# Optimization experiments

Hardware: AMD Instinct MI355X
Metric: run time of the kernel (lower is better)

Reference implementation:

```python
import jax, jax.numpy as jnp
import numpy as np

ALPHA = 0.0

def setup_inputs() -> dict:
    key = jax.random.key(0)
    k1, k2, k3 = jax.random.split(key, 3)
    E = 1000000
    num_nodes = 50000
    num_rels = 237
    edge_index = jax.random.randint(k1, (2, E), 0, num_nodes, dtype=jnp.int64)
    edge_type = jax.random.randint(k2, (E,), 0, num_rels, dtype=jnp.int64)
    batch = jax.random.randint(k3, (64, 32, 3), 0, num_rels, dtype=jnp.int64)
    edge_weight = jnp.ones((E,), dtype=jnp.float32)
    return {
        "edge_index": edge_index,
        "edge_type": edge_type,
        "batch": batch,
        "edge_weight": edge_weight,
        "num_nodes": num_nodes,
    }


def reference(edge_index, edge_type, batch, edge_weight, num_nodes):
    # Per query i (row of batch), count tail nodes of training edges whose
    # head == h_index[i,0] and relation == r_index[i,0]; softmax over nodes.
    h = batch[:, 0, 0]  # [B] query head entity
    r = batch[:, 0, 2]  # [B] query relation
    heads = edge_index[0]  # [E]
    tails = edge_index[1]  # [E]
    # [B, E] boolean: which training edges match each query's (head, rel)
    match = (heads[None, :] == h[:, None]) & (edge_type[None, :] == r[:, None])
    contrib = jnp.where(match, edge_weight[None, :], jnp.float32(0.0))  # [B, E]
    B = batch.shape[0]
    # Scatter-add matched edges into per-query tail histograms == bincount
    dist = jnp.zeros((B, num_nodes), dtype=jnp.float32).at[:, tails].add(contrib)
    freq_res = jax.nn.softmax(dist, axis=1)
    return (freq_res, ALPHA)
```

## Files before the change

### kernel.cpp

```cpp
#include <hip/hip_runtime.h>
#include <float.h>
#include <stdint.h>


#define SOFTMAX_BLOCK 1024

__device__ __forceinline__ float waveMax(float v) {
#pragma unroll
    for (int off = 32; off; off >>= 1) v = fmaxf(v, __shfl_down(v, off, 64));
    return v;
}
__device__ __forceinline__ float waveSum(float v) {
#pragma unroll
    for (int off = 32; off; off >>= 1) v += __shfl_down(v, off, 64);
    return v;
}

__global__ void scatter_kernel(const int* __restrict__ edge_index,
                               const int* __restrict__ etype,
                               const float* __restrict__ ew,
                               const int* __restrict__ batch,
                               float* __restrict__ dist,
                               int E, int N, int B) {
    extern __shared__ unsigned s_keys[];
    for (int i = threadIdx.x; i < B; i += blockDim.x) {
        unsigned h = (unsigned)batch[i * 96 + 0];
        unsigned r = (unsigned)batch[i * 96 + 2];
        s_keys[i] = (h << 16) | (r & 0xFFFFu);
    }
    __syncthreads();
    int e = blockIdx.x * blockDim.x + threadIdx.x;
    if (e >= E) return;
    unsigned key = ((unsigned)edge_index[e] << 16) | ((unsigned)etype[e] & 0xFFFFu);
    int tail = -1;
    float w = 0.0f;
    for (int b = 0; b < B; ++b) {
        if (s_keys[b] == key) {
            if (tail < 0) { tail = edge_index[E + e]; w = ew[e]; }
            atomicAdd(dist + (size_t)b * N + tail, w);
        }
    }
}

__global__ __launch_bounds__(SOFTMAX_BLOCK)
void softmax_kernel(float* __restrict__ dist, int N) {
    __shared__ float s_red[SOFTMAX_BLOCK / 64];
    __shared__ float s_bcast;
    const int tid = threadIdx.x;
    const int nw = SOFTMAX_BLOCK / 64;
    float* row = dist + (size_t)blockIdx.x * N;
    const bool vec4 = ((N & 3) == 0) && ((((uintptr_t)row) & 15) == 0);

    float m = -FLT_MAX;
    if (vec4) {
        const float4* row4 = (const float4*)row;
        const int N4 = N >> 2;
        for (int i = tid; i < N4; i += SOFTMAX_BLOCK) {
            float4 v = row4[i];
            m = fmaxf(m, fmaxf(fmaxf(v.x, v.y), fmaxf(v.z, v.w)));
        }
    } else {
        for (int i = tid; i < N; i += SOFTMAX_BLOCK) m = fmaxf(m, row[i]);
    }
    m = waveMax(m);
    if ((tid & 63) == 0) s_red[tid >> 6] = m;
    __syncthreads();
    if (tid < 64) {
        float v = (tid < nw) ? s_red[tid] : -FLT_MAX;
        v = waveMax(v);
        if (tid == 0) s_bcast = v;
    }
    __syncthreads();
    const float M = s_bcast;
    __syncthreads();

    float s = 0.0f;
    if (vec4) {
        const float4* row4 = (const float4*)row;
        const int N4 = N >> 2;
        for (int i = tid; i < N4; i += SOFTMAX_BLOCK) {
            float4 v = row4[i];
            s += __expf(v.x - M) + __expf(v.y - M) + __expf(v.z - M) + __expf(v.w - M);
        }
    } else {
        for (int i = tid; i < N; i += SOFTMAX_BLOCK) s += __expf(row[i] - M);
    }
    s = waveSum(s);
    if ((tid & 63) == 0) s_red[tid >> 6] = s;
    __syncthreads();
    if (tid < 64) {
        float v = (tid < nw) ? s_red[tid] : 0.0f;
        v = waveSum(v);
        if (tid == 0) s_bcast = v;
    }
    __syncthreads();
    const float invS = 1.0f / s_bcast;

    if (vec4) {
        float4* row4 = (float4*)row;
        const int N4 = N >> 2;
        for (int i = tid; i < N4; i += SOFTMAX_BLOCK) {
            float4 v = row4[i];
            v.x = __expf(v.x - M) * invS;
            v.y = __expf(v.y - M) * invS;
            v.z = __expf(v.z - M) * invS;
            v.w = __expf(v.w - M) * invS;
            row4[i] = v;
        }
    } else {
        for (int i = tid; i < N; i += SOFTMAX_BLOCK) row[i] = __expf(row[i] - M) * invS;
    }
}

extern "C" void kernel_launch(void* const* d_in, const int* in_sizes, int n_in,
                              void* d_out, int out_size, void* d_ws, size_t ws_size,
                              hipStream_t stream) {
    const int*   edge_index = (const int*)d_in[0];
    const int*   edge_type  = (const int*)d_in[1];
    const int*   batch      = (const int*)d_in[2];
    const float* ew         = (const float*)d_in[3];

    const int E = in_sizes[1];
    const int B = in_sizes[2] / 96;
    const int N = (out_size - 1) / B;

    float* out = (float*)d_out;

    hipMemsetAsync(d_out, 0, (size_t)out_size * sizeof(float), stream);

    const int threads = 256;
    const int blocks = (E + threads - 1) / threads;
    scatter_kernel<<<blocks, threads, B * sizeof(unsigned), stream>>>(
        edge_index, edge_type, ew, batch, out, E, N, B);

    softmax_kernel<<<B, SOFTMAX_BLOCK, 0, stream>>>(out, N);
}
```

Before: 100.6 us.

## Compute softmax sparsely from a list of nonzero histogram entries with bloom prefilter

The scatter now records each first-touched (query, tail) cell in a compact list and uses a shared-memory bloom filter plus 4-wide vectorized loads to skip the per-query key scan for most edges. The dense three-pass row softmax is replaced by a single-block stats kernel. It derives each row's max and sum from the listed nonzeros and treats all other cells as zeros. A fill kernel writes the constant background value, and a fixup kernel patches in the nonzero entries. This removes the full-row read passes. In exchange it relies on nonnegative accumulated weights, since the max is seeded at zero and a cell counts as new only when the old value was zero. It also needs a workspace-sized list and silently drops entries if that list overflows.

```diff
diff --git a/kernel.cpp b/kernel.cpp
--- a/kernel.cpp
+++ b/kernel.cpp
@@ -1,115 +1,136 @@
 #include <hip/hip_runtime.h>
-#include <float.h>
 #include <stdint.h>
 
 
-#define SOFTMAX_BLOCK 1024
+#define B_MAX 64
 
-__device__ __forceinline__ float waveMax(float v) {
-#pragma unroll
-    for (int off = 32; off; off >>= 1) v = fmaxf(v, __shfl_down(v, off, 64));
-    return v;
-}
-__device__ __forceinline__ float waveSum(float v) {
-#pragma unroll
-    for (int off = 32; off; off >>= 1) v += __shfl_down(v, off, 64);
-    return v;
-}
-
-__global__ void scatter_kernel(const int* __restrict__ edge_index,
-                               const int* __restrict__ etype,
-                               const float* __restrict__ ew,
-                               const int* __restrict__ batch,
-                               float* __restrict__ dist,
-                               int E, int N, int B) {
-    extern __shared__ unsigned s_keys[];
-    for (int i = threadIdx.x; i < B; i += blockDim.x) {
-        unsigned h = (unsigned)batch[i * 96 + 0];
-        unsigned r = (unsigned)batch[i * 96 + 2];
-        s_keys[i] = (h << 16) | (r & 0xFFFFu);
+__global__ __launch_bounds__(256)
+void scatter_kernel(const int* __restrict__ heads,
+                    const int* __restrict__ tails,
+                    const int* __restrict__ etype,
+                    const float* __restrict__ ew,
+                    const int* __restrict__ batch,
+                    float* __restrict__ dist,
+                    int* __restrict__ cnt,
+                    int2* __restrict__ list,
+                    int E, int N, int B, int listCap) {
+    __shared__ unsigned s_keys[B_MAX];
+    __shared__ unsigned s_bloom[128];
+    if (threadIdx.x < 128) s_bloom[threadIdx.x] = 0u;
+    __syncthreads();
+    if (threadIdx.x < B) {
+        unsigned h = (unsigned)batch[threadIdx.x * 96 + 0];
+        unsigned r = (unsigned)batch[threadIdx.x * 96 + 2];
+        unsigned key = (h << 16) | (r & 0xFFFFu);
+        s_keys[threadIdx.x] = key;
+        unsigned hsh = (key * 0x9E3779B1u) >> 20;
+        atomicOr(&s_bloom[hsh >> 5], 1u << (hsh & 31));
     }
     __syncthreads();
-    int e = blockIdx.x * blockDim.x + threadIdx.x;
-    if (e >= E) return;
-    unsigned key = ((unsigned)edge_index[e] << 16) | ((unsigned)etype[e] & 0xFFFFu);
-    int tail = -1;
-    float w = 0.0f;
-    for (int b = 0; b < B; ++b) {
-        if (s_keys[b] == key) {
-            if (tail < 0) { tail = edge_index[E + e]; w = ew[e]; }
-            atomicAdd(dist + (size_t)b * N + tail, w);
+
+    int base = (blockIdx.x * blockDim.x + threadIdx.x) * 4;
+    if (base >= E) return;
+
+    int h4[4], t4[4];
+    if (base + 3 < E) {
+        int4 hv = ((const int4*)heads)[base >> 2];
+        int4 tv = ((const int4*)etype)[base >> 2];
+        h4[0] = hv.x; h4[1] = hv.y; h4[2] = hv.z; h4[3] = hv.w;
+        t4[0] = tv.x; t4[1] = tv.y; t4[2] = tv.z; t4[3] = tv.w;
+    } else {
+        for (int j = 0; j < 4; ++j) {
+            int e = base + j;
+            h4[j] = (e < E) ? heads[e] : -1;
+            t4[j] = (e < E) ? etype[e] : -1;
+        }
+    }
+#pragma unroll
+    for (int j = 0; j < 4; ++j) {
+        int e = base + j;
+        if (e >= E) break;
+        unsigned key = ((unsigned)h4[j] << 16) | ((unsigned)t4[j] & 0xFFFFu);
+        unsigned hsh = (key * 0x9E3779B1u) >> 20;
+        if (!(s_bloom[hsh >> 5] & (1u << (hsh & 31)))) continue;
+        int tail = -1; float w = 0.0f;
+        for (int b = 0; b < B; ++b) {
+            if (s_keys[b] == key) {
+                if (tail < 0) { tail = tails[e]; w = ew[e]; }
+                float old = atomicAdd(dist + (size_t)b * N + tail, w);
+                if (old == 0.0f) {
+                    int pos = atomicAdd(cnt, 1);
+                    if (pos < listCap) list[pos] = make_int2(b, tail);
+                }
+            }
         }
     }
 }
 
-__global__ __launch_bounds__(SOFTMAX_BLOCK)
-void softmax_kernel(float* __restrict__ dist, int N) {
-    __shared__ float s_red[SOFTMAX_BLOCK / 64];
-    __shared__ float s_bcast;
-    const int tid = threadIdx.x;
-    const int nw = SOFTMAX_BLOCK / 64;
-    float* row = dist + (size_t)blockIdx.x * N;
-    const bool vec4 = ((N & 3) == 0) && ((((uintptr_t)row) & 15) == 0);
-
-    float m = -FLT_MAX;
-    if (vec4) {
-        const float4* row4 = (const float4*)row;
-        const int N4 = N >> 2;
-        for (int i = tid; i < N4; i += SOFTMAX_BLOCK) {
-            float4 v = row4[i];
-            m = fmaxf(m, fmaxf(fmaxf(v.x, v.y), fmaxf(v.z, v.w)));
-        }
-    } else {
-        for (int i = tid; i < N; i += SOFTMAX_BLOCK) m = fmaxf(m, row[i]);
-    }
-    m = waveMax(m);
-    if ((tid & 63) == 0) s_red[tid >> 6] = m;
+__global__ __launch_bounds__(256)
+void stats_kernel(const float* __restrict__ dist,
+                  const int* __restrict__ cnt,
+                  const int2* __restrict__ list,
+                  float* __restrict__ stats,
+                  int N, int B, int listCap) {
+    __shared__ unsigned sM[B_MAX];
+    __shared__ int sCnt[B_MAX];
+    __shared__ float sS[B_MAX];
+    int tid = threadIdx.x;
+    if (tid < B) { sM[tid] = 0u; sCnt[tid] = 0; sS[tid] = 0.0f; }
     __syncthreads();
-    if (tid < 64) {
-        float v = (tid < nw) ? s_red[tid] : -FLT_MAX;
-        v = waveMax(v);
-        if (tid == 0) s_bcast = v;
+    int n = min(*cnt, listCap);
+    for (int i = tid; i < n; i += blockDim.x) {
+        int2 p = list[i];
+        float v = dist[(size_t)p.x * N + p.y];
+        atomicMax(&sM[p.x], __float_as_uint(v));
+        atomicAdd(&sCnt[p.x], 1);
     }
     __syncthreads();
-    const float M = s_bcast;
-    __syncthreads();
-
-    float s = 0.0f;
-    if (vec4) {
-        const float4* row4 = (const float4*)row;
-        const int N4 = N >> 2;
-        for (int i = tid; i < N4; i += SOFTMAX_BLOCK) {
-            float4 v = row4[i];
-            s += __expf(v.x - M) + __expf(v.y - M) + __expf(v.z - M) + __expf(v.w - M);
-        }
-    } else {
-        for (int i = tid; i < N; i += SOFTMAX_BLOCK) s += __expf(row[i] - M);
-    }
-    s = waveSum(s);
-    if ((tid & 63) == 0) s_red[tid >> 6] = s;
-    __syncthreads();
-    if (tid < 64) {
-        float v = (tid < nw) ? s_red[tid] : 0.0f;
-        v = waveSum(v);
-        if (tid == 0) s_bcast = v;
+    for (int i = tid; i < n; i += blockDim.x) {
+        int2 p = list[i];
+        float v = dist[(size_t)p.x * N + p.y];
+        atomicAdd(&sS[p.x], __expf(v - __uint_as_float(sM[p.x])));
     }
     __syncthreads();
-    const float invS = 1.0f / s_bcast;
+    if (tid < B) {
+        float M = __uint_as_float(sM[tid]);
+        float em = __expf(-M);
+        float S = (float)(N - sCnt[tid]) * em + sS[tid];
+        float inv = 1.0f / S;
+        stats[tid]         = M;
+        stats[B + tid]     = inv;
+        stats[2 * B + tid] = em * inv;
+    }
+}
 
-    if (vec4) {
-        float4* row4 = (float4*)row;
-        const int N4 = N >> 2;
-        for (int i = tid; i < N4; i += SOFTMAX_BLOCK) {
-            float4 v = row4[i];
-            v.x = __expf(v.x - M) * invS;
-            v.y = __expf(v.y - M) * invS;
-            v.z = __expf(v.z - M) * invS;
-            v.w = __expf(v.w - M) * invS;
-            row4[i] = v;
-        }
-    } else {
-        for (int i = tid; i < N; i += SOFTMAX_BLOCK) row[i] = __expf(row[i] - M) * invS;
+__global__ __launch_bounds__(256)
+void fill_kernel(float* __restrict__ out, const float* __restrict__ stats,
+                 int N4, int B) {
+    int b = blockIdx.y;
+    float base = stats[2 * B + b];
+    int i = blockIdx.x * blockDim.x + threadIdx.x;
+    if (i < N4) {
+        float4 v = make_float4(base, base, base, base);
+        ((float4*)(out + (size_t)b * (size_t)N4 * 4))[i] = v;
     }
+}
+
+__global__ __launch_bounds__(256)
+void fixup_kernel(float* __restrict__ out, const float* __restrict__ dist,
+                  const float* __restrict__ stats, const int* __restrict__ cnt,
+                  const int2* __restrict__ list, int N, int B, int listCap) {
+    int n = min(*cnt, listCap);
+    int tid = threadIdx.x;
+    for (int i = tid; i < n; i += blockDim.x) {
+        int2 p = list[i];
+        float v = dist[(size_t)p.x * N + p.y];
+        out[(size_t)p.x * N + p.y] = __expf(v - stats[p.x]) * stats[B + p.x];
+    }
+    int tail = N & 3;
+    for (int i = tid; i < tail * B; i += blockDim.x) {
+        int b = i / tail, k = i % tail;
+        out[(size_t)b * N + (N - tail) + k] = stats[2 * B + b];
+    }
+    if (tid == 0) out[(size_t)B * N] = 0.0f;
 }
 
 extern "C" void kernel_launch(void* const* d_in, const int* in_sizes, int n_in,
@@ -123,15 +144,31 @@
     const int E = in_sizes[1];
     const int B = in_sizes[2] / 96;
     const int N = (out_size - 1) / B;
-
     float* out = (float*)d_out;
 
-    hipMemsetAsync(d_out, 0, (size_t)out_size * sizeof(float), stream);
+    char* ws = (char*)d_ws;
+    size_t distBytes = (size_t)B * N * sizeof(float);
+    float* dist  = (float*)ws;
+    float* stats = (float*)(ws + distBytes);
+    int*   cnt   = (int*)(ws + distBytes + (size_t)3 * B * sizeof(float));
+    size_t listOff = distBytes + (size_t)3 * B * sizeof(float) + sizeof(int);
+    listOff = (listOff + 7) & ~(size_t)7;
+    int2* list = (int2*)(ws + listOff);
+    int listCap = (int)((ws_size - listOff) / sizeof(int2));
 
-    const int threads = 256;
-    const int blocks = (E + threads - 1) / threads;
-    scatter_kernel<<<blocks, threads, B * sizeof(unsigned), stream>>>(
-        edge_index, edge_type, ew, batch, out, E, N, B);
+    hipMemsetAsync(d_ws, 0, listOff, stream);
 
-    softmax_kernel<<<B, SOFTMAX_BLOCK, 0, stream>>>(out, N);
+    int threads = 256;
+    int blocks = ((E + 3) / 4 + threads - 1) / threads;
+    scatter_kernel<<<blocks, threads, 0, stream>>>(
+        edge_index, edge_index + E, edge_type, ew, batch,
+        dist, cnt, list, E, N, B, listCap);
+
+    stats_kernel<<<1, 256, 0, stream>>>(dist, cnt, list, stats, N, B, listCap);
+
+    int N4 = N / 4;
+    dim3 fgrid((N4 + 255) / 256, B);
+    fill_kernel<<<fgrid, 256, 0, stream>>>(out, stats, N4, B);
+
+    fixup_kernel<<<1, 256, 0, stream>>>(out, dist, stats, cnt, list, N, B, listCap);
 }
```

New measurement: 105.1 us. 4.6% more time.
